# Performance work log

Measured on AMD Instinct MI355X. Metric: run time of the kernel, lower is better.

Reference implementation:

```python
import jax, jax.numpy as jnp
import numpy as np

H, D = 4, 32          # num_heads, per-head dim (hid_size = 128)
NEG_SLOPE = 0.2


def edge_gat(h_src, h_dst, e_feat, src, dst, W, We, al, ar, ae):
    """DGL-style EdgeGATConv, eval mode (no dropout, no bias/residual).
    h_src:[Ns,F] h_dst:[Nd,F] e_feat:[E,Fe] src/dst:[E] int indices.
    Returns [Nd, H*D]."""
    n_dst = h_dst.shape[0]
    fs = (h_src @ W).reshape(-1, H, D)              # [Ns,H,D]
    fd = (h_dst @ W).reshape(-1, H, D)              # [Nd,H,D]
    fe = (e_feat @ We).reshape(-1, H, D)            # [E,H,D]
    el = (fs * al).sum(-1)                          # [Ns,H]
    er = (fd * ar).sum(-1)                          # [Nd,H]
    ee = (fe * ae).sum(-1)                          # [E,H]
    e = jax.nn.leaky_relu(el[src] + er[dst] + ee, NEG_SLOPE)   # [E,H]
    m = jax.ops.segment_max(e, dst, num_segments=n_dst)       # [Nd,H]
    m = jax.lax.stop_gradient(jnp.where(jnp.isfinite(m), m, 0.0))
    w = jnp.exp(e - m[dst])                                     # [E,H]
    s = jax.ops.segment_sum(w, dst, num_segments=n_dst)         # [Nd,H]
    msg = jax.ops.segment_sum(w[:, :, None] * fs[src], dst, num_segments=n_dst)
    out = msg / (s[:, :, None] + 1e-9)                          # [Nd,H,D]
    return out.reshape(n_dst, H * D)


def setup_inputs() -> dict:
    key = jax.random.key(0)
    N_U = N_I = 50000
    E = 500000
    F_IN, F_E, HID = 128, 16, 128
    ks = iter(jax.random.split(key, 64))
    nk = lambda: next(ks)
    d = {}
    d["X_user"] = jax.random.normal(nk(), (N_U, F_IN), jnp.float32)
    d["X_item"] = jax.random.normal(nk(), (N_I, F_IN), jnp.float32)
    for l in (0, 1):
        for et in ("ui", "iu"):
            d[f"Ef_{et}{l}"] = jax.random.normal(nk(), (E, F_E), jnp.float32)
    for l in (0, 1):
        for et in ("ui", "iu"):
            in_dim = F_IN if l == 0 else HID
            d[f"W_{et}{l}"] = jax.random.normal(nk(), (in_dim, HID), jnp.float32) * in_dim ** -0.5
            d[f"We_{et}{l}"] = jax.random.normal(nk(), (F_E, HID), jnp.float32) * F_E ** -0.5
            for a in ("al", "ar", "ae"):
                d[f"{a}_{et}{l}"] = jax.random.normal(nk(), (H, D), jnp.float32) * 0.1
    d["src_ui"] = jax.random.randint(nk(), (E,), 0, N_U)
    d["dst_ui"] = jax.random.randint(nk(), (E,), 0, N_I)
    d["src_iu"] = jax.random.randint(nk(), (E,), 0, N_I)
    d["dst_iu"] = jax.random.randint(nk(), (E,), 0, N_U)
    return d


def reference(X_user, X_item, Ef_ui0, Ef_iu0, Ef_ui1, Ef_iu1,
              W_ui0, We_ui0, al_ui0, ar_ui0, ae_ui0,
              W_iu0, We_iu0, al_iu0, ar_iu0, ae_iu0,
              W_ui1, We_ui1, al_ui1, ar_ui1, ae_ui1,
              W_iu1, We_iu1, al_iu1, ar_iu1, ae_iu1,
              src_ui, dst_ui, src_iu, dst_iu):
    # ---- layer 0 ----
    hi1 = edge_gat(X_user, X_item, Ef_ui0, src_ui, dst_ui, W_ui0, We_ui0, al_ui0, ar_ui0, ae_ui0)
    hu1 = edge_gat(X_item, X_user, Ef_iu0, src_iu, dst_iu, W_iu0, We_iu0, al_iu0, ar_iu0, ae_iu0)
    # inter-layer relu (+ dropout, identity in eval mode)
    hu1 = jax.nn.relu(hu1)
    hi1 = jax.nn.relu(hi1)
    # ---- layer 1 (last: no relu/dropout) ----
    hi2 = edge_gat(hu1, hi1, Ef_ui1, src_ui, dst_ui, W_ui1, We_ui1, al_ui1, ar_ui1, ae_ui1)
    hu2 = edge_gat(hi1, hu1, Ef_iu1, src_iu, dst_iu, W_iu1, We_iu1, al_iu1, ar_iu1, ae_iu1)
    return (hu2, hi2)
```

## Files before the change

kernel.cpp:

```cpp
#include <hip/hip_runtime.h>
#include <cstdint>

#define HH 4
#define DD 32
#define HID 128
#define FE 16
#define NEG 0.2f

__global__ void k_zero_i32(int* __restrict__ p, int n) {
  int i = blockIdx.x * blockDim.x + threadIdx.x;
  if (i < n) p[i] = 0;
}

__device__ inline unsigned short f2b(float x) {
  unsigned int u = __float_as_uint(x);
  u = (u + 0x7fffu + ((u >> 16) & 1u)) >> 16;
  return (unsigned short)u;
}
__device__ inline float b2f(unsigned short b) {
  return __uint_as_float(((unsigned int)b) << 16);
}

__global__ void k_hist(const int* __restrict__ dst, int* __restrict__ cnt, int E) {
  int i = blockIdx.x * blockDim.x + threadIdx.x;
  if (i < E) atomicAdd(&cnt[dst[i]], 1);
}

__global__ void k_scanA(int* __restrict__ cnt, int* __restrict__ bsum, int N) {
  __shared__ int sh[256];
  int t = threadIdx.x, i = blockIdx.x * 256 + t;
  int v = (i < N) ? cnt[i] : 0;
  sh[t] = v;
  __syncthreads();
  for (int off = 1; off < 256; off <<= 1) {
    int add = (t >= off) ? sh[t - off] : 0;
    __syncthreads();
    sh[t] += add;
    __syncthreads();
  }
  if (i < N) cnt[i] = sh[t];
  if (t == 255) bsum[blockIdx.x] = sh[255];
}

__global__ void k_scanB(int* __restrict__ bsum, int nb) {
  __shared__ int sh[256];
  int t = threadIdx.x;
  int v = (t < nb) ? bsum[t] : 0;
  sh[t] = v;
  __syncthreads();
  for (int off = 1; off < 256; off <<= 1) {
    int add = (t >= off) ? sh[t - off] : 0;
    __syncthreads();
    sh[t] += add;
    __syncthreads();
  }
  if (t < nb) bsum[t] = sh[t] - v;
}

__global__ void k_scanC(const int* __restrict__ cnt, const int* __restrict__ bsum,
                        int* __restrict__ rowptr, int N) {
  int i = blockIdx.x * blockDim.x + threadIdx.x;
  if (i < N) rowptr[i + 1] = cnt[i] + bsum[i >> 8];
  if (i == 0) rowptr[0] = 0;
}

__global__ void k_scatter(const int* __restrict__ dst, const int* __restrict__ src,
                          const int* __restrict__ rowptr, int* __restrict__ fill,
                          int* __restrict__ eidx, int* __restrict__ srcs, int E) {
  int i = blockIdx.x * blockDim.x + threadIdx.x;
  if (i < E) {
    int d = dst[i];
    int pos = rowptr[d] + atomicAdd(&fill[d], 1);
    eidx[pos] = i;
    srcs[pos] = src[i];
  }
}

struct VJob { const float* W; const float* a; float* V; int K; };
struct VJobs { VJob j[6]; };

__global__ void k_makev(VJobs P) {
  VJob job = P.j[blockIdx.x];
  int t = threadIdx.x;
  if (t < job.K) {
    for (int h = 0; h < HH; ++h) {
      const float* wrow = job.W + t * HID + h * DD;
      const float* ar = job.a + h * DD;
      float s = 0.f;
      for (int d = 0; d < DD; ++d) s += wrow[d] * ar[d];
      job.V[t * HH + h] = s;
    }
  }
}

__global__ void k_proj(const float* __restrict__ X, const float* __restrict__ Vl,
                       const float* __restrict__ Vr, float* __restrict__ P, int N) {
  int idx = blockIdx.x * blockDim.x + threadIdx.x;
  if (idx >= N * 8) return;
  int n = idx >> 3, j = idx & 7;
  const float* V = (j < 4) ? Vl : Vr;
  int jj = j & 3;
  const float4* x4 = (const float4*)(X + (size_t)n * HID);
  float acc = 0.f;
#pragma unroll 8
  for (int k4 = 0; k4 < 32; ++k4) {
    float4 x = x4[k4];
    acc += x.x * V[(k4 * 4 + 0) * 4 + jj];
    acc += x.y * V[(k4 * 4 + 1) * 4 + jj];
    acc += x.z * V[(k4 * 4 + 2) * 4 + jj];
    acc += x.w * V[(k4 * 4 + 3) * 4 + jj];
  }
  P[idx] = acc;
}

__global__ void k_ee(const float* __restrict__ Ef, const float* __restrict__ Ve,
                     const int* __restrict__ eidx, float* __restrict__ eec, int E) {
  int j = blockIdx.x * blockDim.x + threadIdx.x;
  if (j >= E) return;
  int e = eidx[j];
  const float4* f4 = (const float4*)(Ef + (size_t)e * FE);
  float a0 = 0.f, a1 = 0.f, a2 = 0.f, a3 = 0.f;
#pragma unroll
  for (int k4 = 0; k4 < 4; ++k4) {
    float4 x = f4[k4];
    const float* v = Ve + k4 * 16;
    a0 += x.x * v[0] + x.y * v[4] + x.z * v[8]  + x.w * v[12];
    a1 += x.x * v[1] + x.y * v[5] + x.z * v[9]  + x.w * v[13];
    a2 += x.x * v[2] + x.y * v[6] + x.z * v[10] + x.w * v[14];
    a3 += x.x * v[3] + x.y * v[7] + x.z * v[11] + x.w * v[15];
  }
  ((float4*)eec)[j] = make_float4(a0, a1, a2, a3);
}

#define BM 64
#define KC 64
__global__ __launch_bounds__(256) void k_gemm(const float* __restrict__ X,
                                              const float* __restrict__ W,
                                              unsigned short* __restrict__ outb, int N) {
  __shared__ float Xs[BM * KC];
  __shared__ float Ws[KC * HID];
  int t = threadIdx.x;
  int bm = blockIdx.x * BM;
  int rg = t >> 5;
  int cg = t & 31;
  float acc[8][4] = {};
  for (int kc = 0; kc < HID; kc += KC) {
    for (int i = t; i < BM * KC / 4; i += 256) {
      int r = i / (KC / 4);
      int c4 = i % (KC / 4);
      int gr = bm + r;
      if (gr >= N) gr = N - 1;
      ((float4*)Xs)[r * (KC / 4) + c4] = *(const float4*)(X + (size_t)gr * HID + kc + c4 * 4);
    }
    for (int i = t; i < KC * HID / 4; i += 256) {
      ((float4*)Ws)[i] = *(const float4*)(W + kc * HID + i * 4);
    }
    __syncthreads();
#pragma unroll 8
    for (int k = 0; k < KC; ++k) {
      float b0 = Ws[k * HID + cg];
      float b1 = Ws[k * HID + cg + 32];
      float b2 = Ws[k * HID + cg + 64];
      float b3 = Ws[k * HID + cg + 96];
#pragma unroll
      for (int i = 0; i < 8; ++i) {
        float a = Xs[(rg * 8 + i) * KC + k];
        acc[i][0] += a * b0;
        acc[i][1] += a * b1;
        acc[i][2] += a * b2;
        acc[i][3] += a * b3;
      }
    }
    __syncthreads();
  }
#pragma unroll
  for (int i = 0; i < 8; ++i) {
    int gr = bm + rg * 8 + i;
    if (gr < N) {
      unsigned short* o = outb + (size_t)gr * HID;
      o[cg]      = f2b(acc[i][0]);
      o[cg + 32] = f2b(acc[i][1]);
      o[cg + 64] = f2b(acc[i][2]);
      o[cg + 96] = f2b(acc[i][3]);
    }
  }
}

template <bool RELU>
__global__ __launch_bounds__(256) void k_agg(
    const int* __restrict__ rowptr, const int* __restrict__ srcs,
    const float* __restrict__ Psrc, const float* __restrict__ Pdst,
    const float* __restrict__ eec, const unsigned short* __restrict__ fsb,
    float* __restrict__ out, int N) {
  int wid = threadIdx.x >> 6;
  int lane = threadIdx.x & 63;
  int n = blockIdx.x * 4 + wid;
  if (n >= N) return;
  int L = lane & 31;
  int h = L >> 3;
  int base = rowptr[n], end = rowptr[n + 1];
  float er = Pdst[n * 8 + 4 + h];
  float s = 0.f, a0 = 0.f, a1 = 0.f, a2 = 0.f, a3 = 0.f;
  int j = base + (lane >> 5);
  int sn = (j < end) ? srcs[j] : 0;
  while (j < end) {
    int jn = j + 2;
    int sn_next = (jn < end) ? srcs[jn] : 0;
    float x = Psrc[sn * 8 + h] + er + eec[j * 4 + h];
    x = (x > 0.f) ? x : NEG * x;
    ushort4 f = *(const ushort4*)(fsb + (size_t)sn * HID + L * 4);
    float w = __expf(x);
    s += w;
    a0 += w * b2f(f.x);
    a1 += w * b2f(f.y);
    a2 += w * b2f(f.z);
    a3 += w * b2f(f.w);
    j = jn;
    sn = sn_next;
  }
  s  += __shfl_xor(s, 32);
  a0 += __shfl_xor(a0, 32);
  a1 += __shfl_xor(a1, 32);
  a2 += __shfl_xor(a2, 32);
  a3 += __shfl_xor(a3, 32);
  if (lane < 32) {
    float inv = 1.f / (s + 1e-9f);
    a0 *= inv; a1 *= inv; a2 *= inv; a3 *= inv;
    if (RELU) {
      a0 = fmaxf(a0, 0.f); a1 = fmaxf(a1, 0.f);
      a2 = fmaxf(a2, 0.f); a3 = fmaxf(a3, 0.f);
    }
    *(float4*)(out + (size_t)n * HID + L * 4) = make_float4(a0, a1, a2, a3);
  }
}

extern "C" void kernel_launch(void* const* d_in, const int* in_sizes, int n_in,
                              void* d_out, int out_size, void* d_ws, size_t ws_size,
                              hipStream_t stream) {
  const float* X_user = (const float*)d_in[0];
  const float* X_item = (const float*)d_in[1];
  const float* Ef_ui[2] = {(const float*)d_in[2], (const float*)d_in[4]};
  const float* Ef_iu[2] = {(const float*)d_in[3], (const float*)d_in[5]};
  const float* Wp[2][2];  const float* Wep[2][2];
  const float* alp[2][2]; const float* arp[2][2]; const float* aep[2][2];
  for (int l = 0; l < 2; ++l)
    for (int et = 0; et < 2; ++et) {
      int b = 6 + (l * 2 + et) * 5;
      Wp[l][et]  = (const float*)d_in[b + 0];
      Wep[l][et] = (const float*)d_in[b + 1];
      alp[l][et] = (const float*)d_in[b + 2];
      arp[l][et] = (const float*)d_in[b + 3];
      aep[l][et] = (const float*)d_in[b + 4];
    }
  const int* src_ui = (const int*)d_in[26];
  const int* dst_ui = (const int*)d_in[27];
  const int* src_iu = (const int*)d_in[28];
  const int* dst_iu = (const int*)d_in[29];

  const int N = in_sizes[0] / HID;
  const int E = in_sizes[26];

  char* w = (char*)d_ws;
  size_t off = 0;
  auto carve = [&](size_t bytes) {
    off = (off + 255) & ~(size_t)255;
    char* p = w + off;
    off += bytes;
    return p;
  };
  int* rowptr_ui = (int*)carve((N + 1) * 4);
  int* rowptr_iu = (int*)carve((N + 1) * 4);
  int* eidx_ui = (int*)carve((size_t)E * 4);
  int* eidx_iu = (int*)carve((size_t)E * 4);
  int* srcs_ui = (int*)carve((size_t)E * 4);
  int* srcs_iu = (int*)carve((size_t)E * 4);
  int* cnt_blk = (int*)carve((size_t)4 * N * 4);
  int* cnt_ui = cnt_blk, *cnt_iu = cnt_blk + N, *fill_ui = cnt_blk + 2 * N, *fill_iu = cnt_blk + 3 * N;
  int* bsum_ui = (int*)carve(256 * 4);
  int* bsum_iu = (int*)carve(256 * 4);
  float* P_user = (float*)carve((size_t)N * 8 * 4);
  float* P_item = (float*)carve((size_t)N * 8 * 4);
  float* eec_ui = (float*)carve((size_t)E * 4 * 4);
  float* eec_iu = (float*)carve((size_t)E * 4 * 4);
  unsigned short* fs_a = (unsigned short*)carve((size_t)N * HID * 2);
  unsigned short* fs_b = (unsigned short*)carve((size_t)N * HID * 2);
  float* h_u1 = (float*)carve((size_t)N * HID * 4);
  float* h_i1 = (float*)carve((size_t)N * HID * 4);
  float* Vl_u = (float*)carve(HID * 4 * 4);
  float* Vr_u = (float*)carve(HID * 4 * 4);
  float* Vl_i = (float*)carve(HID * 4 * 4);
  float* Vr_i = (float*)carve(HID * 4 * 4);
  float* Ve_ui = (float*)carve(FE * 4 * 4);
  float* Ve_iu = (float*)carve(FE * 4 * 4);

  const int nbE = (E + 255) / 256;
  const int nbN = (N + 255) / 256;

  k_zero_i32<<<(4 * N + 255) / 256, 256, 0, stream>>>(cnt_blk, 4 * N);
  k_hist<<<nbE, 256, 0, stream>>>(dst_ui, cnt_ui, E);
  k_hist<<<nbE, 256, 0, stream>>>(dst_iu, cnt_iu, E);
  k_scanA<<<nbN, 256, 0, stream>>>(cnt_ui, bsum_ui, N);
  k_scanA<<<nbN, 256, 0, stream>>>(cnt_iu, bsum_iu, N);
  k_scanB<<<1, 256, 0, stream>>>(bsum_ui, nbN);
  k_scanB<<<1, 256, 0, stream>>>(bsum_iu, nbN);
  k_scanC<<<nbN, 256, 0, stream>>>(cnt_ui, bsum_ui, rowptr_ui, N);
  k_scanC<<<nbN, 256, 0, stream>>>(cnt_iu, bsum_iu, rowptr_iu, N);
  k_scatter<<<nbE, 256, 0, stream>>>(dst_ui, src_ui, rowptr_ui, fill_ui, eidx_ui, srcs_ui, E);
  k_scatter<<<nbE, 256, 0, stream>>>(dst_iu, src_iu, rowptr_iu, fill_iu, eidx_iu, srcs_iu, E);

  for (int l = 0; l < 2; ++l) {
    const float* Xu = (l == 0) ? X_user : h_u1;
    const float* Xi = (l == 0) ? X_item : h_i1;
    VJobs jb;
    jb.j[0] = {Wp[l][0], alp[l][0], Vl_u, HID};
    jb.j[1] = {Wp[l][1], arp[l][1], Vr_u, HID};
    jb.j[2] = {Wp[l][1], alp[l][1], Vl_i, HID};
    jb.j[3] = {Wp[l][0], arp[l][0], Vr_i, HID};
    jb.j[4] = {Wep[l][0], aep[l][0], Ve_ui, FE};
    jb.j[5] = {Wep[l][1], aep[l][1], Ve_iu, FE};
    k_makev<<<6, 128, 0, stream>>>(jb);

    k_proj<<<(N * 8 + 255) / 256, 256, 0, stream>>>(Xu, Vl_u, Vr_u, P_user, N);
    k_proj<<<(N * 8 + 255) / 256, 256, 0, stream>>>(Xi, Vl_i, Vr_i, P_item, N);
    k_ee<<<nbE, 256, 0, stream>>>(Ef_ui[l], Ve_ui, eidx_ui, eec_ui, E);
    k_ee<<<nbE, 256, 0, stream>>>(Ef_iu[l], Ve_iu, eidx_iu, eec_iu, E);
    k_gemm<<<(N + BM - 1) / BM, 256, 0, stream>>>(Xu, Wp[l][0], fs_a, N);
    k_gemm<<<(N + BM - 1) / BM, 256, 0, stream>>>(Xi, Wp[l][1], fs_b, N);

    float* out_ui = (l == 0) ? h_i1 : ((float*)d_out + (size_t)N * HID);
    float* out_iu = (l == 0) ? h_u1 : (float*)d_out;
    int aggGrid = (N + 3) / 4;
    if (l == 0) {
      k_agg<true><<<aggGrid, 256, 0, stream>>>(rowptr_ui, srcs_ui, P_user, P_item,
                                               eec_ui, fs_a, out_ui, N);
      k_agg<true><<<aggGrid, 256, 0, stream>>>(rowptr_iu, srcs_iu, P_item, P_user,
                                               eec_iu, fs_b, out_iu, N);
    } else {
      k_agg<false><<<aggGrid, 256, 0, stream>>>(rowptr_ui, srcs_ui, P_user, P_item,
                                                eec_ui, fs_a, out_ui, N);
      k_agg<false><<<aggGrid, 256, 0, stream>>>(rowptr_iu, srcs_iu, P_item, P_user,
                                                eec_iu, fs_b, out_iu, N);
    }
  }
}
```

Baseline: 763.3 us.

## Batch paired kernels via 2D grids, bf16 intermediates, wider agg gathers, retiled GEMM

Pairs of per-edge-type kernels (hist, scan, scatter, proj, ee, gemm, agg) are merged into single launches using blockIdx.y to select the job. This halves launch count and lets both jobs share the GPU. Layer-0 hidden outputs are stored as bf16 instead of fp32, with bf16-reading variants of proj and gemm, to cut memory traffic. The aggregation kernel now has each lane load 8 bf16 features and processes 4 edges in parallel per wave, with a prefetched gather. The GEMM uses a smaller K chunk and float4 LDS reads. The extra bf16 rounding of intermediates adds precision loss.

```diff
diff --git a/kernel.cpp b/kernel.cpp
--- a/kernel.cpp
+++ b/kernel.cpp
@@ -17,16 +17,21 @@
   u = (u + 0x7fffu + ((u >> 16) & 1u)) >> 16;
   return (unsigned short)u;
 }
-__device__ inline float b2f(unsigned short b) {
-  return __uint_as_float(((unsigned int)b) << 16);
-}
-
-__global__ void k_hist(const int* __restrict__ dst, int* __restrict__ cnt, int E) {
+__device__ inline float lo2f(unsigned int p) { return __uint_as_float(p << 16); }
+__device__ inline float hi2f(unsigned int p) { return __uint_as_float(p & 0xffff0000u); }
+
+__global__ void k_hist2(const int* __restrict__ d0, const int* __restrict__ d1,
+                        int* __restrict__ c0, int* __restrict__ c1, int E) {
+  const int* dst = blockIdx.y ? d1 : d0;
+  int* cnt = blockIdx.y ? c1 : c0;
   int i = blockIdx.x * blockDim.x + threadIdx.x;
   if (i < E) atomicAdd(&cnt[dst[i]], 1);
 }
 
-__global__ void k_scanA(int* __restrict__ cnt, int* __restrict__ bsum, int N) {
+__global__ void k_scanA2(int* __restrict__ c0, int* __restrict__ c1,
+                         int* __restrict__ b0, int* __restrict__ b1, int N) {
+  int* cnt = blockIdx.y ? c1 : c0;
+  int* bsum = blockIdx.y ? b1 : b0;
   __shared__ int sh[256];
   int t = threadIdx.x, i = blockIdx.x * 256 + t;
   int v = (i < N) ? cnt[i] : 0;
@@ -42,7 +47,8 @@
   if (t == 255) bsum[blockIdx.x] = sh[255];
 }
 
-__global__ void k_scanB(int* __restrict__ bsum, int nb) {
+__global__ void k_scanB2(int* __restrict__ b0, int* __restrict__ b1, int nb) {
+  int* bsum = blockIdx.y ? b1 : b0;
   __shared__ int sh[256];
   int t = threadIdx.x;
   int v = (t < nb) ? bsum[t] : 0;
@@ -57,22 +63,30 @@
   if (t < nb) bsum[t] = sh[t] - v;
 }
 
-__global__ void k_scanC(const int* __restrict__ cnt, const int* __restrict__ bsum,
-                        int* __restrict__ rowptr, int N) {
+__global__ void k_scanC2(const int* __restrict__ c0, const int* __restrict__ c1,
+                         const int* __restrict__ b0, const int* __restrict__ b1,
+                         int* __restrict__ r0, int* __restrict__ r1, int N) {
+  const int* cnt = blockIdx.y ? c1 : c0;
+  const int* bsum = blockIdx.y ? b1 : b0;
+  int* rowptr = blockIdx.y ? r1 : r0;
   int i = blockIdx.x * blockDim.x + threadIdx.x;
   if (i < N) rowptr[i + 1] = cnt[i] + bsum[i >> 8];
   if (i == 0) rowptr[0] = 0;
 }
 
-__global__ void k_scatter(const int* __restrict__ dst, const int* __restrict__ src,
-                          const int* __restrict__ rowptr, int* __restrict__ fill,
-                          int* __restrict__ eidx, int* __restrict__ srcs, int E) {
+struct ScatArgs {
+  const int* dst; const int* src; const int* rowptr;
+  int* fill; int* eidx; int* srcs;
+};
+
+__global__ void k_scatter2(ScatArgs s0, ScatArgs s1, int E) {
+  ScatArgs S = blockIdx.y ? s1 : s0;
   int i = blockIdx.x * blockDim.x + threadIdx.x;
   if (i < E) {
-    int d = dst[i];
-    int pos = rowptr[d] + atomicAdd(&fill[d], 1);
-    eidx[pos] = i;
-    srcs[pos] = src[i];
+    int d = S.dst[i];
+    int pos = S.rowptr[d] + atomicAdd(&S.fill[d], 1);
+    S.eidx[pos] = i;
+    S.srcs[pos] = S.src[i];
   }
 }
 
@@ -93,28 +107,52 @@
   }
 }
 
-__global__ void k_proj(const float* __restrict__ X, const float* __restrict__ Vl,
-                       const float* __restrict__ Vr, float* __restrict__ P, int N) {
+template <bool BIN>
+__global__ void k_proj2(const void* __restrict__ X0, const float* __restrict__ Vl0,
+                        const float* __restrict__ Vr0, float* __restrict__ P0,
+                        const void* __restrict__ X1, const float* __restrict__ Vl1,
+                        const float* __restrict__ Vr1, float* __restrict__ P1, int N) {
+  const void* X = blockIdx.y ? X1 : X0;
+  const float* Vl = blockIdx.y ? Vl1 : Vl0;
+  const float* Vr = blockIdx.y ? Vr1 : Vr0;
+  float* P = blockIdx.y ? P1 : P0;
   int idx = blockIdx.x * blockDim.x + threadIdx.x;
   if (idx >= N * 8) return;
   int n = idx >> 3, j = idx & 7;
   const float* V = (j < 4) ? Vl : Vr;
   int jj = j & 3;
-  const float4* x4 = (const float4*)(X + (size_t)n * HID);
   float acc = 0.f;
+  if (BIN) {
+    const unsigned short* xp = (const unsigned short*)X + (size_t)n * HID;
+#pragma unroll
+    for (int c = 0; c < 16; ++c) {
+      uint4 u = *(const uint4*)(xp + c * 8);
+      const float* vb = V + c * 8 * 4 + jj;
+      acc += lo2f(u.x) * vb[0]  + hi2f(u.x) * vb[4];
+      acc += lo2f(u.y) * vb[8]  + hi2f(u.y) * vb[12];
+      acc += lo2f(u.z) * vb[16] + hi2f(u.z) * vb[20];
+      acc += lo2f(u.w) * vb[24] + hi2f(u.w) * vb[28];
+    }
+  } else {
+    const float4* x4 = (const float4*)((const float*)X + (size_t)n * HID);
 #pragma unroll 8
-  for (int k4 = 0; k4 < 32; ++k4) {
-    float4 x = x4[k4];
-    acc += x.x * V[(k4 * 4 + 0) * 4 + jj];
-    acc += x.y * V[(k4 * 4 + 1) * 4 + jj];
-    acc += x.z * V[(k4 * 4 + 2) * 4 + jj];
-    acc += x.w * V[(k4 * 4 + 3) * 4 + jj];
+    for (int k4 = 0; k4 < 32; ++k4) {
+      float4 x = x4[k4];
+      const float* vb = V + k4 * 16 + jj;
+      acc += x.x * vb[0] + x.y * vb[4] + x.z * vb[8] + x.w * vb[12];
+    }
   }
   P[idx] = acc;
 }
 
-__global__ void k_ee(const float* __restrict__ Ef, const float* __restrict__ Ve,
-                     const int* __restrict__ eidx, float* __restrict__ eec, int E) {
+__global__ void k_ee2(const float* __restrict__ Ef0, const float* __restrict__ Ve0,
+                      const int* __restrict__ ei0, float* __restrict__ ec0,
+                      const float* __restrict__ Ef1, const float* __restrict__ Ve1,
+                      const int* __restrict__ ei1, float* __restrict__ ec1, int E) {
+  const float* Ef = blockIdx.y ? Ef1 : Ef0;
+  const float* Ve = blockIdx.y ? Ve1 : Ve0;
+  const int* eidx = blockIdx.y ? ei1 : ei0;
+  float* eec = blockIdx.y ? ec1 : ec0;
   int j = blockIdx.x * blockDim.x + threadIdx.x;
   if (j >= E) return;
   int e = eidx[j];
@@ -133,42 +171,65 @@
 }
 
 #define BM 64
-#define KC 64
-__global__ __launch_bounds__(256) void k_gemm(const float* __restrict__ X,
-                                              const float* __restrict__ W,
-                                              unsigned short* __restrict__ outb, int N) {
-  __shared__ float Xs[BM * KC];
-  __shared__ float Ws[KC * HID];
+#define KC 32
+template <bool BIN>
+__global__ __launch_bounds__(256) void k_gemm2(
+    const void* __restrict__ X0, const float* __restrict__ W0, unsigned short* __restrict__ o0,
+    const void* __restrict__ X1, const float* __restrict__ W1, unsigned short* __restrict__ o1,
+    int N) {
+  const void* X = blockIdx.y ? X1 : X0;
+  const float* W = blockIdx.y ? W1 : W0;
+  unsigned short* outb = blockIdx.y ? o1 : o0;
+  __shared__ float Xs[BM][KC];
+  __shared__ float Ws[KC][HID];
   int t = threadIdx.x;
   int bm = blockIdx.x * BM;
   int rg = t >> 5;
   int cg = t & 31;
   float acc[8][4] = {};
   for (int kc = 0; kc < HID; kc += KC) {
-    for (int i = t; i < BM * KC / 4; i += 256) {
-      int r = i / (KC / 4);
-      int c4 = i % (KC / 4);
-      int gr = bm + r;
-      if (gr >= N) gr = N - 1;
-      ((float4*)Xs)[r * (KC / 4) + c4] = *(const float4*)(X + (size_t)gr * HID + kc + c4 * 4);
-    }
+    if (BIN) {
+      int r = t >> 2, c8 = (t & 3) * 8;
+      int gr = bm + r; if (gr >= N) gr = N - 1;
+      uint4 u = *(const uint4*)((const unsigned short*)X + (size_t)gr * HID + kc + c8);
+      float* xr = &Xs[r][c8];
+      xr[0] = lo2f(u.x); xr[1] = hi2f(u.x);
+      xr[2] = lo2f(u.y); xr[3] = hi2f(u.y);
+      xr[4] = lo2f(u.z); xr[5] = hi2f(u.z);
+      xr[6] = lo2f(u.w); xr[7] = hi2f(u.w);
+    } else {
+#pragma unroll
+      for (int i = t; i < BM * KC / 4; i += 256) {
+        int r = i >> 3, c4 = (i & 7) * 4;
+        int gr = bm + r; if (gr >= N) gr = N - 1;
+        *(float4*)&Xs[r][c4] = *(const float4*)((const float*)X + (size_t)gr * HID + kc + c4);
+      }
+    }
+#pragma unroll
     for (int i = t; i < KC * HID / 4; i += 256) {
-      ((float4*)Ws)[i] = *(const float4*)(W + kc * HID + i * 4);
-    }
-    __syncthreads();
-#pragma unroll 8
-    for (int k = 0; k < KC; ++k) {
-      float b0 = Ws[k * HID + cg];
-      float b1 = Ws[k * HID + cg + 32];
-      float b2 = Ws[k * HID + cg + 64];
-      float b3 = Ws[k * HID + cg + 96];
+      int r = i >> 5, c4 = (i & 31) * 4;
+      *(float4*)&Ws[r][c4] = *(const float4*)(W + (size_t)(kc + r) * HID + c4);
+    }
+    __syncthreads();
+#pragma unroll
+    for (int k4 = 0; k4 < KC / 4; ++k4) {
+      float bv[4][4];
+#pragma unroll
+      for (int kk = 0; kk < 4; ++kk) {
+        bv[kk][0] = Ws[k4 * 4 + kk][cg];
+        bv[kk][1] = Ws[k4 * 4 + kk][cg + 32];
+        bv[kk][2] = Ws[k4 * 4 + kk][cg + 64];
+        bv[kk][3] = Ws[k4 * 4 + kk][cg + 96];
+      }
 #pragma unroll
       for (int i = 0; i < 8; ++i) {
-        float a = Xs[(rg * 8 + i) * KC + k];
-        acc[i][0] += a * b0;
-        acc[i][1] += a * b1;
-        acc[i][2] += a * b2;
-        acc[i][3] += a * b3;
+        float4 a4 = *(const float4*)&Xs[rg * 8 + i][k4 * 4];
+        float av[4] = {a4.x, a4.y, a4.z, a4.w};
+#pragma unroll
+        for (int kk = 0; kk < 4; ++kk)
+#pragma unroll
+          for (int jj = 0; jj < 4; ++jj)
+            acc[i][jj] += av[kk] * bv[kk][jj];
       }
     }
     __syncthreads();
@@ -186,51 +247,77 @@
   }
 }
 
-template <bool RELU>
-__global__ __launch_bounds__(256) void k_agg(
-    const int* __restrict__ rowptr, const int* __restrict__ srcs,
-    const float* __restrict__ Psrc, const float* __restrict__ Pdst,
-    const float* __restrict__ eec, const unsigned short* __restrict__ fsb,
-    float* __restrict__ out, int N) {
+struct AggArgs {
+  const int* rowptr; const int* srcs;
+  const float* Ps; const float* Pd; const float* eec;
+  const unsigned short* fsb; void* out;
+};
+
+template <bool FINAL>
+__global__ __launch_bounds__(256) void k_agg2(AggArgs a0, AggArgs a1, int N) {
+  AggArgs A = blockIdx.y ? a1 : a0;
   int wid = threadIdx.x >> 6;
   int lane = threadIdx.x & 63;
   int n = blockIdx.x * 4 + wid;
   if (n >= N) return;
-  int L = lane & 31;
-  int h = L >> 3;
-  int base = rowptr[n], end = rowptr[n + 1];
-  float er = Pdst[n * 8 + 4 + h];
-  float s = 0.f, a0 = 0.f, a1 = 0.f, a2 = 0.f, a3 = 0.f;
-  int j = base + (lane >> 5);
-  int sn = (j < end) ? srcs[j] : 0;
+  int q = lane >> 4;
+  int L = lane & 15;
+  int h = L >> 2;
+  int base = A.rowptr[n], end = A.rowptr[n + 1];
+  float er = A.Pd[n * 8 + 4 + h];
+  float s = 0.f;
+  float c0 = 0.f, c1 = 0.f, c2 = 0.f, c3 = 0.f, c4 = 0.f, c5 = 0.f, c6 = 0.f, c7 = 0.f;
+  int j = base + q;
+  int sn = 0;
+  uint4 f = {};
+  if (j < end) {
+    sn = A.srcs[j];
+    f = *(const uint4*)(A.fsb + (size_t)sn * HID + L * 8);
+  }
   while (j < end) {
-    int jn = j + 2;
-    int sn_next = (jn < end) ? srcs[jn] : 0;
-    float x = Psrc[sn * 8 + h] + er + eec[j * 4 + h];
+    int jn = j + 4;
+    int snn = 0;
+    uint4 g = {};
+    if (jn < end) {
+      snn = A.srcs[jn];
+      g = *(const uint4*)(A.fsb + (size_t)snn * HID + L * 8);
+    }
+    float x = A.Ps[sn * 8 + h] + er + A.eec[j * 4 + h];
     x = (x > 0.f) ? x : NEG * x;
-    ushort4 f = *(const ushort4*)(fsb + (size_t)sn * HID + L * 4);
     float w = __expf(x);
     s += w;
-    a0 += w * b2f(f.x);
-    a1 += w * b2f(f.y);
-    a2 += w * b2f(f.z);
-    a3 += w * b2f(f.w);
-    j = jn;
-    sn = sn_next;
-  }
-  s  += __shfl_xor(s, 32);
-  a0 += __shfl_xor(a0, 32);
-  a1 += __shfl_xor(a1, 32);
-  a2 += __shfl_xor(a2, 32);
-  a3 += __shfl_xor(a3, 32);
-  if (lane < 32) {
+    c0 += w * lo2f(f.x); c1 += w * hi2f(f.x);
+    c2 += w * lo2f(f.y); c3 += w * hi2f(f.y);
+    c4 += w * lo2f(f.z); c5 += w * hi2f(f.z);
+    c6 += w * lo2f(f.w); c7 += w * hi2f(f.w);
+    j = jn; sn = snn; f = g;
+  }
+  s  += __shfl_xor(s, 16);  s  += __shfl_xor(s, 32);
+  c0 += __shfl_xor(c0, 16); c0 += __shfl_xor(c0, 32);
+  c1 += __shfl_xor(c1, 16); c1 += __shfl_xor(c1, 32);
+  c2 += __shfl_xor(c2, 16); c2 += __shfl_xor(c2, 32);
+  c3 += __shfl_xor(c3, 16); c3 += __shfl_xor(c3, 32);
+  c4 += __shfl_xor(c4, 16); c4 += __shfl_xor(c4, 32);
+  c5 += __shfl_xor(c5, 16); c5 += __shfl_xor(c5, 32);
+  c6 += __shfl_xor(c6, 16); c6 += __shfl_xor(c6, 32);
+  c7 += __shfl_xor(c7, 16); c7 += __shfl_xor(c7, 32);
+  if (lane < 16) {
     float inv = 1.f / (s + 1e-9f);
-    a0 *= inv; a1 *= inv; a2 *= inv; a3 *= inv;
-    if (RELU) {
-      a0 = fmaxf(a0, 0.f); a1 = fmaxf(a1, 0.f);
-      a2 = fmaxf(a2, 0.f); a3 = fmaxf(a3, 0.f);
-    }
-    *(float4*)(out + (size_t)n * HID + L * 4) = make_float4(a0, a1, a2, a3);
+    c0 *= inv; c1 *= inv; c2 *= inv; c3 *= inv;
+    c4 *= inv; c5 *= inv; c6 *= inv; c7 *= inv;
+    if (FINAL) {
+      float* op = (float*)A.out + (size_t)n * HID + L * 8;
+      *(float4*)op = make_float4(c0, c1, c2, c3);
+      *(float4*)(op + 4) = make_float4(c4, c5, c6, c7);
+    } else {
+      c0 = fmaxf(c0, 0.f); c1 = fmaxf(c1, 0.f); c2 = fmaxf(c2, 0.f); c3 = fmaxf(c3, 0.f);
+      c4 = fmaxf(c4, 0.f); c5 = fmaxf(c5, 0.f); c6 = fmaxf(c6, 0.f); c7 = fmaxf(c7, 0.f);
+      unsigned short* op = (unsigned short*)A.out + (size_t)n * HID + L * 8;
+      ushort4 u0 = {f2b(c0), f2b(c1), f2b(c2), f2b(c3)};
+      ushort4 u1 = {f2b(c4), f2b(c5), f2b(c6), f2b(c7)};
+      *(ushort4*)op = u0;
+      *(ushort4*)(op + 4) = u1;
+    }
   }
 }
 
@@ -284,8 +371,8 @@
   float* eec_iu = (float*)carve((size_t)E * 4 * 4);
   unsigned short* fs_a = (unsigned short*)carve((size_t)N * HID * 2);
   unsigned short* fs_b = (unsigned short*)carve((size_t)N * HID * 2);
-  float* h_u1 = (float*)carve((size_t)N * HID * 4);
-  float* h_i1 = (float*)carve((size_t)N * HID * 4);
+  unsigned short* h_u1 = (unsigned short*)carve((size_t)N * HID * 2);
+  unsigned short* h_i1 = (unsigned short*)carve((size_t)N * HID * 2);
   float* Vl_u = (float*)carve(HID * 4 * 4);
   float* Vr_u = (float*)carve(HID * 4 * 4);
   float* Vl_i = (float*)carve(HID * 4 * 4);
@@ -295,22 +382,20 @@
 
   const int nbE = (E + 255) / 256;
   const int nbN = (N + 255) / 256;
+  dim3 g2E(nbE, 2), g2N(nbN, 2);
 
   k_zero_i32<<<(4 * N + 255) / 256, 256, 0, stream>>>(cnt_blk, 4 * N);
-  k_hist<<<nbE, 256, 0, stream>>>(dst_ui, cnt_ui, E);
-  k_hist<<<nbE, 256, 0, stream>>>(dst_iu, cnt_iu, E);
-  k_scanA<<<nbN, 256, 0, stream>>>(cnt_ui, bsum_ui, N);
-  k_scanA<<<nbN, 256, 0, stream>>>(cnt_iu, bsum_iu, N);
-  k_scanB<<<1, 256, 0, stream>>>(bsum_ui, nbN);
-  k_scanB<<<1, 256, 0, stream>>>(bsum_iu, nbN);
-  k_scanC<<<nbN, 256, 0, stream>>>(cnt_ui, bsum_ui, rowptr_ui, N);
-  k_scanC<<<nbN, 256, 0, stream>>>(cnt_iu, bsum_iu, rowptr_iu, N);
-  k_scatter<<<nbE, 256, 0, stream>>>(dst_ui, src_ui, rowptr_ui, fill_ui, eidx_ui, srcs_ui, E);
-  k_scatter<<<nbE, 256, 0, stream>>>(dst_iu, src_iu, rowptr_iu, fill_iu, eidx_iu, srcs_iu, E);
+  k_hist2<<<g2E, 256, 0, stream>>>(dst_ui, dst_iu, cnt_ui, cnt_iu, E);
+  k_scanA2<<<g2N, 256, 0, stream>>>(cnt_ui, cnt_iu, bsum_ui, bsum_iu, N);
+  k_scanB2<<<dim3(1, 2), 256, 0, stream>>>(bsum_ui, bsum_iu, nbN);
+  k_scanC2<<<g2N, 256, 0, stream>>>(cnt_ui, cnt_iu, bsum_ui, bsum_iu, rowptr_ui, rowptr_iu, N);
+  ScatArgs s0 = {dst_ui, src_ui, rowptr_ui, fill_ui, eidx_ui, srcs_ui};
+  ScatArgs s1 = {dst_iu, src_iu, rowptr_iu, fill_iu, eidx_iu, srcs_iu};
+  k_scatter2<<<g2E, 256, 0, stream>>>(s0, s1, E);
 
   for (int l = 0; l < 2; ++l) {
-    const float* Xu = (l == 0) ? X_user : h_u1;
-    const float* Xi = (l == 0) ? X_item : h_i1;
+    const void* Xu = (l == 0) ? (const void*)X_user : (const void*)h_u1;
+    const void* Xi = (l == 0) ? (const void*)X_item : (const void*)h_i1;
     VJobs jb;
     jb.j[0] = {Wp[l][0], alp[l][0], Vl_u, HID};
     jb.j[1] = {Wp[l][1], arp[l][1], Vr_u, HID};
@@ -320,26 +405,30 @@
     jb.j[5] = {Wep[l][1], aep[l][1], Ve_iu, FE};
     k_makev<<<6, 128, 0, stream>>>(jb);
 
-    k_proj<<<(N * 8 + 255) / 256, 256, 0, stream>>>(Xu, Vl_u, Vr_u, P_user, N);
-    k_proj<<<(N * 8 + 255) / 256, 256, 0, stream>>>(Xi, Vl_i, Vr_i, P_item, N);
-    k_ee<<<nbE, 256, 0, stream>>>(Ef_ui[l], Ve_ui, eidx_ui, eec_ui, E);
-    k_ee<<<nbE, 256, 0, stream>>>(Ef_iu[l], Ve_iu, eidx_iu, eec_iu, E);
-    k_gemm<<<(N + BM - 1) / BM, 256, 0, stream>>>(Xu, Wp[l][0], fs_a, N);
-    k_gemm<<<(N + BM - 1) / BM, 256, 0, stream>>>(Xi, Wp[l][1], fs_b, N);
-
-    float* out_ui = (l == 0) ? h_i1 : ((float*)d_out + (size_t)N * HID);
-    float* out_iu = (l == 0) ? h_u1 : (float*)d_out;
-    int aggGrid = (N + 3) / 4;
+    dim3 gp((N * 8 + 255) / 256, 2);
+    dim3 gg((N + BM - 1) / BM, 2);
+    dim3 ga((N + 3) / 4, 2);
     if (l == 0) {
-      k_agg<true><<<aggGrid, 256, 0, stream>>>(rowptr_ui, srcs_ui, P_user, P_item,
-                                               eec_ui, fs_a, out_ui, N);
-      k_agg<true><<<aggGrid, 256, 0, stream>>>(rowptr_iu, srcs_iu, P_item, P_user,
-                                               eec_iu, fs_b, out_iu, N);
+      k_proj2<false><<<gp, 256, 0, stream>>>(Xu, Vl_u, Vr_u, P_user, Xi, Vl_i, Vr_i, P_item, N);
     } else {
-      k_agg<false><<<aggGrid, 256, 0, stream>>>(rowptr_ui, srcs_ui, P_user, P_item,
-                                                eec_ui, fs_a, out_ui, N);
-      k_agg<false><<<aggGrid, 256, 0, stream>>>(rowptr_iu, srcs_iu, P_item, P_user,
-                                                eec_iu, fs_b, out_iu, N);
-    }
-  }
-}
+      k_proj2<true><<<gp, 256, 0, stream>>>(Xu, Vl_u, Vr_u, P_user, Xi, Vl_i, Vr_i, P_item, N);
+    }
+    k_ee2<<<g2E, 256, 0, stream>>>(Ef_ui[l], Ve_ui, eidx_ui, eec_ui,
+                                   Ef_iu[l], Ve_iu, eidx_iu, eec_iu, E);
+    if (l == 0) {
+      k_gemm2<false><<<gg, 256, 0, stream>>>(Xu, Wp[l][0], fs_a, Xi, Wp[l][1], fs_b, N);
+    } else {
+      k_gemm2<true><<<gg, 256, 0, stream>>>(Xu, Wp[l][0], fs_a, Xi, Wp[l][1], fs_b, N);
+    }
+
+    void* out_ui = (l == 0) ? (void*)h_i1 : (void*)((float*)d_out + (size_t)N * HID);
+    void* out_iu = (l == 0) ? (void*)h_u1 : (void*)d_out;
+    AggArgs aUI = {rowptr_ui, srcs_ui, P_user, P_item, eec_ui, fs_a, out_ui};
+    AggArgs aIU = {rowptr_iu, srcs_iu, P_item, P_user, eec_iu, fs_b, out_iu};
+    if (l == 0) {
+      k_agg2<false><<<ga, 256, 0, stream>>>(aUI, aIU, N);
+    } else {
+      k_agg2<true><<<ga, 256, 0, stream>>>(aUI, aIU, N);
+    }
+  }
+}
```

New measurement: 662.1 us. 1.15x faster.
